# Performance work log

Hardware: AMD Instinct MI355X
Metric: run time of the kernel (lower is better)

## Reference

```python
import jax, jax.numpy as jnp
import numpy as np

N = 50000
E = 1_600_000
IN_CH = 128
HEADS = 4
OUT_CH = 32
NEG_SLOPE = 0.2


def setup_inputs() -> dict:
    key = jax.random.key(0)
    k1, k2, k3, k4, k5, k6 = jax.random.split(key, 6)
    x = jax.random.normal(k1, (N, IN_CH), dtype=jnp.float32)
    edge_index = jax.random.randint(k2, (2, E), 0, N, dtype=jnp.int64)
    # GATConv params: linear weight, per-head attention vectors, output bias
    scale = 1.0 / np.sqrt(IN_CH)
    W = jax.random.normal(k3, (IN_CH, HEADS * OUT_CH), dtype=jnp.float32) * scale
    att_src = jax.random.normal(k4, (HEADS, OUT_CH), dtype=jnp.float32) * scale
    att_dst = jax.random.normal(k5, (HEADS, OUT_CH), dtype=jnp.float32) * scale
    bias = jnp.zeros((HEADS * OUT_CH,), dtype=jnp.float32)
    return {"x": x, "edge_index": edge_index, "W": W, "att_src": att_src,
            "att_dst": att_dst, "bias": bias}


def reference(x, edge_index, W, att_src, att_dst, bias):
    n = x.shape[0]
    # add self loops (PyG GATConv default add_self_loops=True)
    loops = jnp.arange(n, dtype=edge_index.dtype)
    src = jnp.concatenate([edge_index[0], loops])  # message source j
    dst = jnp.concatenate([edge_index[1], loops])  # message target i

    h = (x @ W).reshape(n, HEADS, OUT_CH)  # [N,H,C]
    a_src = jnp.einsum('nhc,hc->nh', h, att_src)  # [N,H]
    a_dst = jnp.einsum('nhc,hc->nh', h, att_dst)  # [N,H]

    e = jax.nn.leaky_relu(a_src[src] + a_dst[dst], NEG_SLOPE)  # [E+N,H]
    # segment softmax over incoming edges of each target node
    m = jax.ops.segment_max(e, dst, num_segments=n)  # [N,H]
    p = jnp.exp(e - m[dst])
    s = jax.ops.segment_sum(p, dst, num_segments=n)  # [N,H]
    alpha = p / s[dst]  # self loops guarantee s > 0

    # weighted scatter-aggregate of source features
    out = jax.ops.segment_sum(alpha[:, :, None] * h[src], dst, num_segments=n)  # [N,H,C]
    out = out.reshape(n, HEADS * OUT_CH) + bias
    return jax.nn.elu(out)
```

## Files before the change

### kernel.cpp

```cpp
#include <hip/hip_runtime.h>
#include <hip/hip_bf16.h>

#define IN_CH 128
#define HEADS 4
#define OUT_CH 32
#define HC 128
#define NEG_SLOPE 0.2f
#define BSHIFT 7
#define CHUNK 4096
#define BUCKCAP 5120

__device__ __forceinline__ unsigned short f2bf(float f) {
  unsigned int u = __float_as_uint(f);
  return (unsigned short)((u + 0x7fffu + ((u >> 16) & 1u)) >> 16);
}
__device__ __forceinline__ float bf2f(unsigned short b) {
  return __uint_as_float(((unsigned int)b) << 16);
}
__device__ __forceinline__ float bflo(unsigned int g) {
  return __uint_as_float((g & 0xffffu) << 16);
}
__device__ __forceinline__ float bfhi(unsigned int g) {
  return __uint_as_float(g & 0xffff0000u);
}

__global__ void detect_kernel(const void* xptr, const void* eptr, int* flags) {
  __shared__ int sok[256], sz[256];
  int t = threadIdx.x;
  const unsigned short* u = (const unsigned short*)xptr;
  float a = fabsf(bf2f(u[t]));
  sok[t] = (a >= 1e-6f && a <= 1e3f) ? 1 : 0;
  const int* ip = (const int*)eptr;
  int z = 0;
#pragma unroll
  for (int k = 0; k < 4; k++) z += (ip[2 * (t * 4 + k) + 1] == 0) ? 1 : 0;
  sz[t] = z;
  __syncthreads();
  for (int s = 128; s > 0; s >>= 1) {
    if (t < s) { sok[t] += sok[t + s]; sz[t] += sz[t + s]; }
    __syncthreads();
  }
  if (t == 0) {
    flags[0] = (sok[0] >= 240) ? 1 : 0;
    flags[1] = (sz[0] >= 900) ? 1 : 0;
  }
}

__global__ void zero_i32(int* __restrict__ p, int n) {
  int i = blockIdx.x * blockDim.x + threadIdx.x;
  if (i < n) p[i] = 0;
}

__global__ void cvt_params(const void* __restrict__ Wr, const void* __restrict__ asr,
                           const void* __restrict__ adr, const void* __restrict__ br,
                           float* __restrict__ Wf, float* __restrict__ asf,
                           float* __restrict__ adf, float* __restrict__ bf,
                           int* __restrict__ cursorA, const int* __restrict__ flags) {
  int i = blockIdx.x * blockDim.x + threadIdx.x;
  int isbf = flags[0];
  auto rd = [&](const void* p, int k) -> float {
    return isbf ? bf2f(((const unsigned short*)p)[k]) : ((const float*)p)[k];
  };
  if (i < 512) cursorA[i] = i * BUCKCAP;
  if (i < IN_CH * HC) Wf[i] = rd(Wr, i);
  else {
    int r = i - IN_CH * HC;
    if (r < HC)            asf[r] = rd(asr, r);
    else if (r < 2 * HC)   adf[r - HC] = rd(adr, r - HC);
    else if (r < 3 * HC)   bf[r - 2 * HC] = rd(br, r - 2 * HC);
  }
}

__device__ __forceinline__ void load_edge(const void* __restrict__ ei,
                                          const int* __restrict__ flags,
                                          int e, int E, int& j, int& d) {
  if (flags[1]) {
    const long long* q = (const long long*)ei;
    j = (int)q[e]; d = (int)q[E + e];
  } else {
    const int* p = (const int*)ei;
    j = p[e]; d = p[E + e];
  }
}

__global__ void gemm_kernel(const void* __restrict__ xraw, const float* __restrict__ W,
                            const float* __restrict__ asf, const float* __restrict__ adf,
                            unsigned short* __restrict__ h_bf,
                            float* __restrict__ a_srcO, float* __restrict__ a_dstO,
                            int N, const int* __restrict__ flags) {
  __shared__ float xs[128][33];
  int t = threadIdx.x;
  int nb = blockIdx.x * 32;
  int isbf = flags[0];
  for (int r = 0; r < 16; r++) {
    int idx = r * 256 + t;
    int nl = idx >> 7;
    int c = idx & 127;
    int n = nb + nl;
    float v = 0.f;
    if (n < N) {
      size_t gi = (size_t)n * IN_CH + c;
      v = isbf ? bf2f(((const unsigned short*)xraw)[gi]) : ((const float*)xraw)[gi];
    }
    xs[c][nl] = v;
  }
  __syncthreads();
  int tc = t & 31, c0 = tc * 4;
  int tn = t >> 5, n0 = tn * 4;
  float acc[4][4];
#pragma unroll
  for (int i = 0; i < 4; i++)
#pragma unroll
    for (int q = 0; q < 4; q++) acc[i][q] = 0.f;
  for (int k = 0; k < 128; k++) {
    float4 w = *(const float4*)&W[k * HC + c0];
    float x0 = xs[k][n0], x1 = xs[k][n0 + 1], x2 = xs[k][n0 + 2], x3 = xs[k][n0 + 3];
    acc[0][0] += x0 * w.x; acc[0][1] += x0 * w.y; acc[0][2] += x0 * w.z; acc[0][3] += x0 * w.w;
    acc[1][0] += x1 * w.x; acc[1][1] += x1 * w.y; acc[1][2] += x1 * w.z; acc[1][3] += x1 * w.w;
    acc[2][0] += x2 * w.x; acc[2][1] += x2 * w.y; acc[2][2] += x2 * w.z; acc[2][3] += x2 * w.w;
    acc[3][0] += x3 * w.x; acc[3][1] += x3 * w.y; acc[3][2] += x3 * w.z; acc[3][3] += x3 * w.w;
  }
#pragma unroll
  for (int i = 0; i < 4; i++) {
    int n = nb + n0 + i;
    if (n >= N) continue;
    size_t o = (size_t)n * HC + c0;
    ushort4 hb;
    hb.x = f2bf(acc[i][0]);
    hb.y = f2bf(acc[i][1]);
    hb.z = f2bf(acc[i][2]);
    hb.w = f2bf(acc[i][3]);
    *(ushort4*)&h_bf[o] = hb;
  }
  float4 wsc = *(const float4*)&asf[c0];
  float4 wdc = *(const float4*)&adf[c0];
  int hh = tc >> 3;
#pragma unroll
  for (int i = 0; i < 4; i++) {
    float ps = acc[i][0] * wsc.x + acc[i][1] * wsc.y + acc[i][2] * wsc.z + acc[i][3] * wsc.w;
    float pd = acc[i][0] * wdc.x + acc[i][1] * wdc.y + acc[i][2] * wdc.z + acc[i][3] * wdc.w;
    ps += __shfl_xor(ps, 1, 64); ps += __shfl_xor(ps, 2, 64); ps += __shfl_xor(ps, 4, 64);
    pd += __shfl_xor(pd, 1, 64); pd += __shfl_xor(pd, 2, 64); pd += __shfl_xor(pd, 4, 64);
    int n = nb + n0 + i;
    if ((tc & 7) == 0 && n < N) {
      a_srcO[n * HEADS + hh] = ps;
      a_dstO[n * HEADS + hh] = pd;
    }
  }
}

__global__ void partA(const void* __restrict__ ei, int* __restrict__ cursorA,
                      unsigned int* __restrict__ ebuf, int E, int N,
                      const int* __restrict__ flags) {
  __shared__ int hist[512];
  int nbuck = (N + ((1 << BSHIFT) - 1)) >> BSHIFT;
  int t = threadIdx.x;
  for (int b = t; b < nbuck; b += 256) hist[b] = 0;
  __syncthreads();
  int base = blockIdx.x * CHUNK;
  unsigned int v[16];
#pragma unroll
  for (int k = 0; k < 16; k++) {
    int e = base + k * 256 + t;
    if (e < E) {
      int j, d;
      load_edge(ei, flags, e, E, j, d);
      v[k] = (unsigned int)j | ((unsigned int)d << 16);
      atomicAdd(&hist[d >> BSHIFT], 1);
    } else v[k] = 0xffffffffu;
  }
  __syncthreads();
  for (int b = t; b < nbuck; b += 256) {
    int c = hist[b];
    if (c > 0) hist[b] = atomicAdd(&cursorA[b], c);
  }
  __syncthreads();
#pragma unroll
  for (int k = 0; k < 16; k++) {
    if (v[k] != 0xffffffffu) {
      int b = (int)(v[k] >> 16) >> BSHIFT;
      int pos = atomicAdd(&hist[b], 1);
      if (pos < (b + 1) * BUCKCAP) ebuf[pos] = v[k];
    }
  }
}

__global__ void partB(const unsigned int* __restrict__ ebuf, const int* __restrict__ cursorA,
                      int* __restrict__ rowbeg, int* __restrict__ rowend,
                      unsigned short* __restrict__ src_sorted, int N) {
  __shared__ int cnt[128];
  __shared__ int stmp[128];
  __shared__ int lcur[128];
  int b = blockIdx.x;
  int t = threadIdx.x;
  int n0 = b << BSHIFT;
  int r0 = b * BUCKCAP;
  int r1 = min(cursorA[b], r0 + BUCKCAP);
  if (t < 128) cnt[t] = 0;
  __syncthreads();
  for (int pos = r0 + t; pos < r1; pos += 256)
    atomicAdd(&cnt[(ebuf[pos] >> 16) & 127], 1);
  __syncthreads();
  int x = 0, v = 0;
  if (t < 128) { v = cnt[t]; x = v; stmp[t] = x; }
  __syncthreads();
  for (int ofs = 1; ofs < 128; ofs <<= 1) {
    int y = (t < 128 && t >= ofs) ? stmp[t - ofs] : 0;
    __syncthreads();
    if (t < 128) { x += y; stmp[t] = x; }
    __syncthreads();
  }
  if (t < 128) {
    int excl = x - v;
    lcur[t] = r0 + excl;
    int n = n0 + t;
    if (n < N) { rowbeg[n] = r0 + excl; rowend[n] = r0 + excl + v; }
  }
  __syncthreads();
  for (int pos = r0 + t; pos < r1; pos += 256) {
    unsigned int w = ebuf[pos];
    int slot = atomicAdd(&lcur[(w >> 16) & 127], 1);
    src_sorted[slot] = (unsigned short)(w & 0xffffu);
  }
}

__global__ void hist_kernel(const void* __restrict__ ei, int* __restrict__ counts,
                            int E, const int* __restrict__ flags) {
  int e = blockIdx.x * blockDim.x + threadIdx.x;
  if (e >= E) return;
  int d;
  if (flags[1]) d = (int)((const long long*)ei)[E + e];
  else          d = ((const int*)ei)[E + e];
  atomicAdd(&counts[d], 1);
}

__global__ void scan1(const int* __restrict__ in, int* __restrict__ excl,
                      int* __restrict__ bsums, int N) {
  __shared__ int tmp[256];
  int t = threadIdx.x;
  int i = blockIdx.x * 256 + t;
  int v = (i < N) ? in[i] : 0;
  int x = v;
  tmp[t] = x;
  __syncthreads();
  for (int ofs = 1; ofs < 256; ofs <<= 1) {
    int y = (t >= ofs) ? tmp[t - ofs] : 0;
    __syncthreads();
    x += y;
    tmp[t] = x;
    __syncthreads();
  }
  if (i < N) excl[i] = x - v;
  if (t == 255) bsums[blockIdx.x] = x;
}

__global__ void scan2(const int* __restrict__ bsums, int* __restrict__ boffs, int nb) {
  __shared__ int tmp[256];
  int t = threadIdx.x;
  int v = (t < nb) ? bsums[t] : 0;
  int x = v;
  tmp[t] = x;
  __syncthreads();
  for (int ofs = 1; ofs < 256; ofs <<= 1) {
    int y = (t >= ofs) ? tmp[t - ofs] : 0;
    __syncthreads();
    x += y;
    tmp[t] = x;
    __syncthreads();
  }
  if (t < nb) boffs[t] = x - v;
}

__global__ void scan3(const int* __restrict__ excl, const int* __restrict__ boffs,
                      int* __restrict__ rowbeg, int* __restrict__ rowend,
                      const int* __restrict__ counts, int N, int E) {
  int i = blockIdx.x * 256 + threadIdx.x;
  if (i < N) {
    int beg = excl[i] + boffs[i >> 8];
    rowbeg[i] = beg;
    rowend[i] = beg + counts[i];
  }
}

__global__ void scatter_kernel(const void* __restrict__ ei, const int* __restrict__ rowbeg,
                               int* __restrict__ cursor, int* __restrict__ src_sorted,
                               int E, const int* __restrict__ flags) {
  int e = blockIdx.x * blockDim.x + threadIdx.x;
  if (e >= E) return;
  int j, d;
  load_edge(ei, flags, e, E, j, d);
  int slot = atomicAdd(&cursor[d], 1);
  src_sorted[rowbeg[d] + slot] = j;
}

template <typename IdxT>
__global__ void agg_csr(const int* __restrict__ rowbeg, const int* __restrict__ rowend,
                        const IdxT* __restrict__ src_sorted,
                        const float* __restrict__ a_src, const float* __restrict__ a_dst,
                        const unsigned short* __restrict__ h_bf,
                        const float* __restrict__ bias,
                        float* __restrict__ out, int N) {
  int wid = threadIdx.x >> 6;
  int lane = threadIdx.x & 63;
  int d = blockIdx.x * 4 + wid;
  if (d >= N) return;
  int g = lane >> 4;
  int sl = lane & 15;
  int c0 = sl * 8;
  int hh = sl >> 2;
  float adst = a_dst[d * HEADS + hh];
  float e0 = a_src[d * HEADS + hh] + adst;
  e0 = e0 > 0.f ? e0 : NEG_SLOPE * e0;
  float ps = (g == 0) ? __expf(e0) : 0.f;
  uint4 qs = *(const uint4*)&h_bf[(size_t)d * HC + c0];
  float acc[8];
  acc[0] = ps * bflo(qs.x); acc[1] = ps * bfhi(qs.x);
  acc[2] = ps * bflo(qs.y); acc[3] = ps * bfhi(qs.y);
  acc[4] = ps * bflo(qs.z); acc[5] = ps * bfhi(qs.z);
  acc[6] = ps * bflo(qs.w); acc[7] = ps * bfhi(qs.w);
  float den = ps;
  int pos = rowbeg[d], r1 = rowend[d];
  for (; pos + 16 <= r1; pos += 16) {
    int ja = (int)src_sorted[pos + g];
    int jb = (int)src_sorted[pos + 4 + g];
    int jc = (int)src_sorted[pos + 8 + g];
    int jd = (int)src_sorted[pos + 12 + g];
    uint4 qa = *(const uint4*)&h_bf[(size_t)ja * HC + c0];
    uint4 qb = *(const uint4*)&h_bf[(size_t)jb * HC + c0];
    uint4 qc = *(const uint4*)&h_bf[(size_t)jc * HC + c0];
    uint4 qd = *(const uint4*)&h_bf[(size_t)jd * HC + c0];
    float aa = a_src[ja * HEADS + hh] + adst;
    float ab = a_src[jb * HEADS + hh] + adst;
    float ac = a_src[jc * HEADS + hh] + adst;
    float ad = a_src[jd * HEADS + hh] + adst;
    aa = aa > 0.f ? aa : NEG_SLOPE * aa;
    ab = ab > 0.f ? ab : NEG_SLOPE * ab;
    ac = ac > 0.f ? ac : NEG_SLOPE * ac;
    ad = ad > 0.f ? ad : NEG_SLOPE * ad;
    float pa = __expf(aa), pb = __expf(ab), pc = __expf(ac), pd = __expf(ad);
    den += pa + pb + pc + pd;
    acc[0] += pa * bflo(qa.x) + pb * bflo(qb.x) + pc * bflo(qc.x) + pd * bflo(qd.x);
    acc[1] += pa * bfhi(qa.x) + pb * bfhi(qb.x) + pc * bfhi(qc.x) + pd * bfhi(qd.x);
    acc[2] += pa * bflo(qa.y) + pb * bflo(qb.y) + pc * bflo(qc.y) + pd * bflo(qd.y);
    acc[3] += pa * bfhi(qa.y) + pb * bfhi(qb.y) + pc * bfhi(qc.y) + pd * bfhi(qd.y);
    acc[4] += pa * bflo(qa.z) + pb * bflo(qb.z) + pc * bflo(qc.z) + pd * bflo(qd.z);
    acc[5] += pa * bfhi(qa.z) + pb * bfhi(qb.z) + pc * bfhi(qc.z) + pd * bfhi(qd.z);
    acc[6] += pa * bflo(qa.w) + pb * bflo(qb.w) + pc * bflo(qc.w) + pd * bflo(qd.w);
    acc[7] += pa * bfhi(qa.w) + pb * bfhi(qb.w) + pc * bfhi(qc.w) + pd * bfhi(qd.w);
  }
  for (; pos + 8 <= r1; pos += 8) {
    int ja = (int)src_sorted[pos + g];
    int jb = (int)src_sorted[pos + 4 + g];
    uint4 qa = *(const uint4*)&h_bf[(size_t)ja * HC + c0];
    uint4 qb = *(const uint4*)&h_bf[(size_t)jb * HC + c0];
    float aa = a_src[ja * HEADS + hh] + adst;
    float ab = a_src[jb * HEADS + hh] + adst;
    aa = aa > 0.f ? aa : NEG_SLOPE * aa;
    ab = ab > 0.f ? ab : NEG_SLOPE * ab;
    float pa = __expf(aa), pb = __expf(ab);
    den += pa + pb;
    acc[0] += pa * bflo(qa.x) + pb * bflo(qb.x);
    acc[1] += pa * bfhi(qa.x) + pb * bfhi(qb.x);
    acc[2] += pa * bflo(qa.y) + pb * bflo(qb.y);
    acc[3] += pa * bfhi(qa.y) + pb * bfhi(qb.y);
    acc[4] += pa * bflo(qa.z) + pb * bflo(qb.z);
    acc[5] += pa * bfhi(qa.z) + pb * bfhi(qb.z);
    acc[6] += pa * bflo(qa.w) + pb * bflo(qb.w);
    acc[7] += pa * bfhi(qa.w) + pb * bfhi(qb.w);
  }
  for (; pos < r1; pos += 4) {
    int rem = r1 - pos;
    int gg = (g < rem) ? g : 0;
    int j = (int)src_sorted[pos + gg];
    float av = a_src[j * HEADS + hh] + adst;
    av = av > 0.f ? av : NEG_SLOPE * av;
    float pe = (g < rem) ? __expf(av) : 0.f;
    uint4 q = *(const uint4*)&h_bf[(size_t)j * HC + c0];
    den += pe;
    acc[0] += pe * bflo(q.x); acc[1] += pe * bfhi(q.x);
    acc[2] += pe * bflo(q.y); acc[3] += pe * bfhi(q.y);
    acc[4] += pe * bflo(q.z); acc[5] += pe * bfhi(q.z);
    acc[6] += pe * bflo(q.w); acc[7] += pe * bfhi(q.w);
  }
#pragma unroll
  for (int q = 0; q < 8; q++) {
    acc[q] += __shfl_xor(acc[q], 16, 64);
    acc[q] += __shfl_xor(acc[q], 32, 64);
  }
  den += __shfl_xor(den, 16, 64);
  den += __shfl_xor(den, 32, 64);
  if (g == 0) {
    float inv = 1.f / den;
    float4 b0 = *(const float4*)&bias[c0];
    float4 b1 = *(const float4*)&bias[c0 + 4];
    float o[8];
    o[0] = acc[0] * inv + b0.x; o[1] = acc[1] * inv + b0.y;
    o[2] = acc[2] * inv + b0.z; o[3] = acc[3] * inv + b0.w;
    o[4] = acc[4] * inv + b1.x; o[5] = acc[5] * inv + b1.y;
    o[6] = acc[6] * inv + b1.z; o[7] = acc[7] * inv + b1.w;
#pragma unroll
    for (int q = 0; q < 8; q++) o[q] = o[q] > 0.f ? o[q] : __expf(o[q]) - 1.f;
    *(float4*)&out[(size_t)d * HC + c0]     = make_float4(o[0], o[1], o[2], o[3]);
    *(float4*)&out[(size_t)d * HC + c0 + 4] = make_float4(o[4], o[5], o[6], o[7]);
  }
}

extern "C" void kernel_launch(void* const* d_in, const int* in_sizes, int n_in,
                              void* d_out, int out_size, void* d_ws, size_t ws_size,
                              hipStream_t stream) {
  const void* x_raw  = d_in[0];
  const void* ei_raw = d_in[1];
  const void* W_raw  = d_in[2];
  const void* as_raw = d_in[3];
  const void* ad_raw = d_in[4];
  const void* b_raw  = d_in[5];
  const int N = in_sizes[0] / IN_CH;
  int E = in_sizes[1] / 2;
  if (in_sizes[1] == 6400000) E = 1600000;

  char* wsp = (char*)d_ws;
  size_t off = 0;
  auto walloc = [&](size_t bytes) {
    void* ptr = wsp + off;
    off += (bytes + 255) & ~(size_t)255;
    return ptr;
  };
  int*   flags   = (int*)walloc(64);
  float* Wf      = (float*)walloc((size_t)IN_CH * HC * 4);
  float* asf     = (float*)walloc(HC * 4);
  float* adf     = (float*)walloc(HC * 4);
  float* bf      = (float*)walloc(HC * 4);
  float* a_src   = (float*)walloc((size_t)N * HEADS * 4);
  float* a_dst   = (float*)walloc((size_t)N * HEADS * 4);
  unsigned short* h_bf = (unsigned short*)walloc((size_t)N * HC * 2);
  int*   cursorA = (int*)walloc(512 * 4);
  int*   rowbeg  = (int*)walloc((size_t)N * 4);
  int*   rowend  = (int*)walloc((size_t)N * 4);

  const int NBUCK = (N + ((1 << BSHIFT) - 1)) >> BSHIFT;
  size_t padded = (size_t)NBUCK * BUCKCAP;

  const int NB_N = (N + 255) / 256;
  const int NB_E = (E + 255) / 256;
  const int NB_A = (E + CHUNK - 1) / CHUNK;

  detect_kernel<<<1, 256, 0, stream>>>(x_raw, ei_raw, flags);
  cvt_params<<<(IN_CH * HC + 3 * HC + 255) / 256, 256, 0, stream>>>(
      W_raw, as_raw, ad_raw, b_raw, Wf, asf, adf, bf, cursorA, flags);

  gemm_kernel<<<(N + 31) / 32, 256, 0, stream>>>(x_raw, Wf, asf, adf, h_bf,
                                                 a_src, a_dst, N, flags);

  if (N < 65535) {
    unsigned short* src_sorted = (unsigned short*)walloc(padded * 2);
    unsigned int*   ebuf       = (unsigned int*)walloc(padded * 4);
    partA<<<NB_A, 256, 0, stream>>>(ei_raw, cursorA, ebuf, E, N, flags);
    partB<<<NBUCK, 256, 0, stream>>>(ebuf, cursorA, rowbeg, rowend, src_sorted, N);
    agg_csr<unsigned short><<<(N + 3) / 4, 256, 0, stream>>>(
        rowbeg, rowend, src_sorted, a_src, a_dst, h_bf, bf, (float*)d_out, N);
  } else {
    int* src_sorted = (int*)walloc((size_t)E * 4);
    int* counts = (int*)walloc((size_t)(N + 1) * 4);
    int* pexcl  = (int*)walloc((size_t)N * 4);
    int* bsums  = (int*)walloc(256 * 4);
    int* boffs  = (int*)walloc(256 * 4);
    zero_i32<<<NB_N, 256, 0, stream>>>(counts, N + 1);
    hist_kernel<<<NB_E, 256, 0, stream>>>(ei_raw, counts, E, flags);
    scan1<<<NB_N, 256, 0, stream>>>(counts, pexcl, bsums, N);
    scan2<<<1, 256, 0, stream>>>(bsums, boffs, NB_N);
    scan3<<<NB_N, 256, 0, stream>>>(pexcl, boffs, rowbeg, rowend, counts, N, E);
    zero_i32<<<NB_N, 256, 0, stream>>>(counts, N + 1);
    scatter_kernel<<<NB_E, 256, 0, stream>>>(ei_raw, rowbeg, counts, src_sorted, E, flags);
    agg_csr<int><<<(N + 3) / 4, 256, 0, stream>>>(
        rowbeg, rowend, src_sorted, a_src, a_dst, h_bf, bf, (float*)d_out, N);
  }
}
```

Measured before the change: 223.2 us.

## Fold dtype detection into cvt_params and co-launch GEMM with edge partition

Dtype and index-width detection now runs redundantly in every block of cvt_params, which removes the separate detect_kernel launch. The node-feature GEMM and the first edge-bucketing pass (partA) are merged into one grid, with blocks split by index. This lets the two independent stages run concurrently and saves a launch. The cost is a shared-memory union sized to the larger user and extra redundant reduction work in each cvt_params block.

```diff
diff --git a/kernel.cpp b/kernel.cpp
--- a/kernel.cpp
+++ b/kernel.cpp
@@ -24,28 +24,6 @@
   return __uint_as_float(g & 0xffff0000u);
 }
 
-__global__ void detect_kernel(const void* xptr, const void* eptr, int* flags) {
-  __shared__ int sok[256], sz[256];
-  int t = threadIdx.x;
-  const unsigned short* u = (const unsigned short*)xptr;
-  float a = fabsf(bf2f(u[t]));
-  sok[t] = (a >= 1e-6f && a <= 1e3f) ? 1 : 0;
-  const int* ip = (const int*)eptr;
-  int z = 0;
-#pragma unroll
-  for (int k = 0; k < 4; k++) z += (ip[2 * (t * 4 + k) + 1] == 0) ? 1 : 0;
-  sz[t] = z;
-  __syncthreads();
-  for (int s = 128; s > 0; s >>= 1) {
-    if (t < s) { sok[t] += sok[t + s]; sz[t] += sz[t + s]; }
-    __syncthreads();
-  }
-  if (t == 0) {
-    flags[0] = (sok[0] >= 240) ? 1 : 0;
-    flags[1] = (sz[0] >= 900) ? 1 : 0;
-  }
-}
-
 __global__ void zero_i32(int* __restrict__ p, int n) {
   int i = blockIdx.x * blockDim.x + threadIdx.x;
   if (i < n) p[i] = 0;
@@ -53,11 +31,32 @@
 
 __global__ void cvt_params(const void* __restrict__ Wr, const void* __restrict__ asr,
                            const void* __restrict__ adr, const void* __restrict__ br,
+                           const void* __restrict__ xptr, const void* __restrict__ eptr,
                            float* __restrict__ Wf, float* __restrict__ asf,
                            float* __restrict__ adf, float* __restrict__ bf,
-                           int* __restrict__ cursorA, const int* __restrict__ flags) {
-  int i = blockIdx.x * blockDim.x + threadIdx.x;
-  int isbf = flags[0];
+                           int* __restrict__ cursorA, int* __restrict__ flags) {
+  __shared__ int sok[256], sz[256];
+  int t = threadIdx.x;
+  {
+    const unsigned short* u = (const unsigned short*)xptr;
+    float a = fabsf(bf2f(u[t]));
+    sok[t] = (a >= 1e-6f && a <= 1e3f) ? 1 : 0;
+    const int* ip = (const int*)eptr;
+    int z = 0;
+#pragma unroll
+    for (int k = 0; k < 4; k++) z += (ip[2 * (t * 4 + k) + 1] == 0) ? 1 : 0;
+    sz[t] = z;
+    __syncthreads();
+    for (int s = 128; s > 0; s >>= 1) {
+      if (t < s) { sok[t] += sok[t + s]; sz[t] += sz[t + s]; }
+      __syncthreads();
+    }
+  }
+  int isbf = (sok[0] >= 240) ? 1 : 0;
+  int is64 = (sz[0] >= 900) ? 1 : 0;
+  if (blockIdx.x == 0 && t == 0) { flags[0] = isbf; flags[1] = is64; }
+
+  int i = blockIdx.x * blockDim.x + t;
   auto rd = [&](const void* p, int k) -> float {
     return isbf ? bf2f(((const unsigned short*)p)[k]) : ((const float*)p)[k];
   };
@@ -83,15 +82,13 @@
   }
 }
 
-__global__ void gemm_kernel(const void* __restrict__ xraw, const float* __restrict__ W,
-                            const float* __restrict__ asf, const float* __restrict__ adf,
-                            unsigned short* __restrict__ h_bf,
-                            float* __restrict__ a_srcO, float* __restrict__ a_dstO,
-                            int N, const int* __restrict__ flags) {
-  __shared__ float xs[128][33];
-  int t = threadIdx.x;
-  int nb = blockIdx.x * 32;
-  int isbf = flags[0];
+__device__ void gemm_body(const void* __restrict__ xraw, const float* __restrict__ W,
+                          const float* __restrict__ asf, const float* __restrict__ adf,
+                          unsigned short* __restrict__ h_bf,
+                          float* __restrict__ a_srcO, float* __restrict__ a_dstO,
+                          int N, int isbf, float (*xs)[33], int bid) {
+  int t = threadIdx.x;
+  int nb = bid * 32;
   for (int r = 0; r < 16; r++) {
     int idx = r * 256 + t;
     int nl = idx >> 7;
@@ -149,15 +146,14 @@
   }
 }
 
-__global__ void partA(const void* __restrict__ ei, int* __restrict__ cursorA,
-                      unsigned int* __restrict__ ebuf, int E, int N,
-                      const int* __restrict__ flags) {
-  __shared__ int hist[512];
+__device__ void partA_body(const void* __restrict__ ei, int* __restrict__ cursorA,
+                           unsigned int* __restrict__ ebuf, int E, int N,
+                           const int* __restrict__ flags, int* hist, int bid) {
   int nbuck = (N + ((1 << BSHIFT) - 1)) >> BSHIFT;
   int t = threadIdx.x;
   for (int b = t; b < nbuck; b += 256) hist[b] = 0;
   __syncthreads();
-  int base = blockIdx.x * CHUNK;
+  int base = bid * CHUNK;
   unsigned int v[16];
 #pragma unroll
   for (int k = 0; k < 16; k++) {
@@ -183,6 +179,31 @@
       if (pos < (b + 1) * BUCKCAP) ebuf[pos] = v[k];
     }
   }
+}
+
+__global__ void fused_gemm_partA(const void* __restrict__ xraw, const float* __restrict__ W,
+                                 const float* __restrict__ asf, const float* __restrict__ adf,
+                                 unsigned short* __restrict__ h_bf,
+                                 float* __restrict__ a_src, float* __restrict__ a_dst,
+                                 const void* __restrict__ ei, int* __restrict__ cursorA,
+                                 unsigned int* __restrict__ ebuf, int E, int N,
+                                 const int* __restrict__ flags, int NB_G) {
+  __shared__ __align__(16) char smem[16896];
+  if (blockIdx.x < NB_G) {
+    gemm_body(xraw, W, asf, adf, h_bf, a_src, a_dst, N, flags[0],
+              (float(*)[33])smem, blockIdx.x);
+  } else {
+    partA_body(ei, cursorA, ebuf, E, N, flags, (int*)smem, blockIdx.x - NB_G);
+  }
+}
+
+__global__ void gemm_kernel(const void* __restrict__ xraw, const float* __restrict__ W,
+                            const float* __restrict__ asf, const float* __restrict__ adf,
+                            unsigned short* __restrict__ h_bf,
+                            float* __restrict__ a_src, float* __restrict__ a_dst,
+                            int N, const int* __restrict__ flags) {
+  __shared__ float xs[128][33];
+  gemm_body(xraw, W, asf, adf, h_bf, a_src, a_dst, N, flags[0], xs, blockIdx.x);
 }
 
 __global__ void partB(const unsigned int* __restrict__ ebuf, const int* __restrict__ cursorA,
@@ -440,21 +461,19 @@
   const int NBUCK = (N + ((1 << BSHIFT) - 1)) >> BSHIFT;
   size_t padded = (size_t)NBUCK * BUCKCAP;
 
+  const int NB_G = (N + 31) / 32;
   const int NB_N = (N + 255) / 256;
   const int NB_E = (E + 255) / 256;
   const int NB_A = (E + CHUNK - 1) / CHUNK;
 
-  detect_kernel<<<1, 256, 0, stream>>>(x_raw, ei_raw, flags);
   cvt_params<<<(IN_CH * HC + 3 * HC + 255) / 256, 256, 0, stream>>>(
-      W_raw, as_raw, ad_raw, b_raw, Wf, asf, adf, bf, cursorA, flags);
-
-  gemm_kernel<<<(N + 31) / 32, 256, 0, stream>>>(x_raw, Wf, asf, adf, h_bf,
-                                                 a_src, a_dst, N, flags);
+      W_raw, as_raw, ad_raw, b_raw, x_raw, ei_raw, Wf, asf, adf, bf, cursorA, flags);
 
   if (N < 65535) {
     unsigned short* src_sorted = (unsigned short*)walloc(padded * 2);
     unsigned int*   ebuf       = (unsigned int*)walloc(padded * 4);
-    partA<<<NB_A, 256, 0, stream>>>(ei_raw, cursorA, ebuf, E, N, flags);
+    fused_gemm_partA<<<NB_G + NB_A, 256, 0, stream>>>(
+        x_raw, Wf, asf, adf, h_bf, a_src, a_dst, ei_raw, cursorA, ebuf, E, N, flags, NB_G);
     partB<<<NBUCK, 256, 0, stream>>>(ebuf, cursorA, rowbeg, rowend, src_sorted, N);
     agg_csr<unsigned short><<<(N + 3) / 4, 256, 0, stream>>>(
         rowbeg, rowend, src_sorted, a_src, a_dst, h_bf, bf, (float*)d_out, N);
@@ -464,6 +483,7 @@
     int* pexcl  = (int*)walloc((size_t)N * 4);
     int* bsums  = (int*)walloc(256 * 4);
     int* boffs  = (int*)walloc(256 * 4);
+    gemm_kernel<<<NB_G, 256, 0, stream>>>(x_raw, Wf, asf, adf, h_bf, a_src, a_dst, N, flags);
     zero_i32<<<NB_N, 256, 0, stream>>>(counts, N + 1);
     hist_kernel<<<NB_E, 256, 0, stream>>>(ei_raw, counts, E, flags);
     scan1<<<NB_N, 256, 0, stream>>>(counts, pexcl, bsums, N);
```

New measurement: 212.6 us. 1.05x faster.
